# Optimization experiments

Measured on AMD Instinct MI355X. Metric: run time of the kernel, lower is better.

## Reference

```python
import jax, jax.numpy as jnp
import numpy as np

N_NODES = 100000
N_EDGES = 1600000
IN_DIM = 512
HID = 32
BN_EPS = 1e-5


def _gcn_layer(x, W, b, src, dst, n_nodes):
    # GCNConv: x' = D^{-1/2} (A + I) D^{-1/2} (x W) + b, degrees include self-loop
    h = x @ W  # [N, H]
    deg = jax.ops.segment_sum(jnp.ones(src.shape[0], x.dtype), dst, num_segments=n_nodes) + 1.0
    dinv = jax.lax.rsqrt(deg)  # [N]
    coef = dinv[src] * dinv[dst]  # [E]
    msg = h[src] * coef[:, None]  # gather + scale, [E, H]
    agg = jax.ops.segment_sum(msg, dst, num_segments=n_nodes)  # scatter-add
    agg = agg + h * (dinv * dinv)[:, None]  # self-loop term
    return agg + b


def setup_inputs() -> dict:
    key = jax.random.key(0)
    ks = jax.random.split(key, 10)
    x = jax.random.normal(ks[0], (N_NODES, IN_DIM), dtype=jnp.float32)
    edge_index = jax.random.randint(ks[1], (2, N_EDGES), 0, N_NODES, dtype=jnp.int32)
    W1 = jax.random.normal(ks[2], (IN_DIM, HID), dtype=jnp.float32) / np.sqrt(IN_DIM)
    b1 = jnp.zeros((HID,), jnp.float32)
    W2 = jax.random.normal(ks[3], (HID, HID), dtype=jnp.float32) / np.sqrt(HID)
    b2 = jnp.zeros((HID,), jnp.float32)
    gamma = jnp.ones((HID,), jnp.float32)
    beta = jnp.zeros((HID,), jnp.float32)
    run_mean = jnp.zeros((HID,), jnp.float32)
    run_var = jnp.ones((HID,), jnp.float32)
    return {"x": x, "edge_index": edge_index, "W1": W1, "b1": b1, "W2": W2,
            "b2": b2, "gamma": gamma, "beta": beta, "run_mean": run_mean, "run_var": run_var}


def reference(x, edge_index, W1, b1, W2, b2, gamma, beta, run_mean, run_var):
    # Eval mode: dropout is identity, BatchNorm uses running stats.
    src, dst = edge_index[0], edge_index[1]
    h = _gcn_layer(x, W1, b1, src, dst, N_NODES)
    h = jax.nn.relu(h)
    h = (h - run_mean) * jax.lax.rsqrt(run_var + BN_EPS) * gamma + beta
    h = _gcn_layer(h, W2, b2, src, dst, N_NODES)
    h = jax.nn.relu(h)
    return h  # post_process is undefined in source -> identity
```

## Files before the change

### kernel.cpp

```cpp
#include <hip/hip_runtime.h>

#define NN 100000
#define NE 1600000
#define IN_DIM 512
#define HID 32
#define BN_EPS 1e-5f

#define E_PER 4
#define FILL_BLOCKS 1600
#define NPASS 25
#define SEG 64

__global__ void k_zero(int* __restrict__ p, int n) {
    int i = blockIdx.x * 256 + threadIdx.x;
    if (i < n) p[i] = 0;
}

__global__ __launch_bounds__(256) void k_fill(const int* __restrict__ src,
                                              const int* __restrict__ dst,
                                              int* __restrict__ cnt,
                                              int* __restrict__ csr, int E, int nthreads) {
    int tid = blockIdx.x * 256 + threadIdx.x;
    int s[E_PER], d[E_PER];
#pragma unroll
    for (int k = 0; k < E_PER; k++) {
        int e = tid + k * nthreads;
        bool ok = (e < E);
        s[k] = ok ? src[e] : 0;
        d[k] = ok ? dst[e] : -1;
    }
    for (int p = 0; p < NPASS; p++) {
#pragma unroll
        for (int k = 0; k < E_PER; k++) {
            if ((d[k] >> 12) == p) {
                int pos = atomicAdd(&cnt[d[k]], 1);
                if (pos < SEG) csr[d[k] * SEG + pos] = s[k];
            }
        }
    }
}

__device__ inline void fma4(float4& a, float s, const float4& w) {
    a.x = fmaf(s, w.x, a.x);
    a.y = fmaf(s, w.y, a.y);
    a.z = fmaf(s, w.z, a.z);
    a.w = fmaf(s, w.w, a.w);
}

#define XS_S 132
__global__ __launch_bounds__(256) void k_gemm1(const float* __restrict__ x,
                                               const float* __restrict__ W,
                                               float* __restrict__ h, int n) {
    __shared__ float XsT[32 * XS_S];
    __shared__ float Ws[32 * 32];
    int t = threadIdx.x;
    int tc = t & 7;
    int tr = t >> 3;
    int base = blockIdx.x * 128;

    float4 acc[4] = {{0,0,0,0},{0,0,0,0},{0,0,0,0},{0,0,0,0}};
    int st_c4 = t & 7, st_row = t >> 3;

    for (int kt = 0; kt < IN_DIM; kt += 32) {
        __syncthreads();
#pragma unroll
        for (int i = 0; i < 4; i++) {
            int row = st_row + i * 32;
            int gr = min(base + row, n - 1);
            float4 v = *(const float4*)(x + (size_t)gr * IN_DIM + kt + (st_c4 << 2));
            XsT[(st_c4 * 4 + 0) * XS_S + row] = v.x;
            XsT[(st_c4 * 4 + 1) * XS_S + row] = v.y;
            XsT[(st_c4 * 4 + 2) * XS_S + row] = v.z;
            XsT[(st_c4 * 4 + 3) * XS_S + row] = v.w;
        }
        *(float4*)&Ws[t * 4] = *(const float4*)(W + kt * HID + t * 4);
        __syncthreads();

#pragma unroll
        for (int kk = 0; kk < 32; kk++) {
            float4 xv = *(const float4*)&XsT[kk * XS_S + tr * 4];
            float4 wv = *(const float4*)&Ws[kk * HID + tc * 4];
            fma4(acc[0], xv.x, wv);
            fma4(acc[1], xv.y, wv);
            fma4(acc[2], xv.z, wv);
            fma4(acc[3], xv.w, wv);
        }
    }
#pragma unroll
    for (int r = 0; r < 4; r++) {
        int row = base + tr * 4 + r;
        if (row < n) *(float4*)(h + (size_t)row * HID + (tc << 2)) = acc[r];
    }
}

__global__ __launch_bounds__(256) void k_agg1(const float* __restrict__ h,
                                              const int* __restrict__ csr,
                                              const int* __restrict__ cnt,
                                              const float* __restrict__ bias,
                                              const float* __restrict__ gamma,
                                              const float* __restrict__ beta,
                                              const float* __restrict__ mean,
                                              const float* __restrict__ var,
                                              float* __restrict__ h2, int n) {
    int t = threadIdx.x;
    int c = t & 31;
    int node = blockIdx.x * 8 + (t >> 5);
    if (node >= n) return;

    int dnode = cnt[node];
    float dn = rsqrtf((float)dnode + 1.0f);
    int d = min(dnode, SEG);
    int o0 = node * SEG;
    float sum = h[(size_t)node * HID + c] * dn;

    for (int ch = 0; ch < d; ch += 32) {
        int rem = d - ch;
        int sv = 0;
        float dv = 0.f;
        if (c < rem) {
            sv = csr[o0 + ch + c];
            dv = rsqrtf((float)cnt[sv] + 1.0f);
        }
        int m = min(rem, 32);
        int mu = (m + 7) & ~7;
        for (int j = 0; j < mu; j += 8) {
            int ss[8];
            float cf[8], v[8];
#pragma unroll
            for (int u = 0; u < 8; u++) {
                ss[u] = __shfl(sv, j + u, 32);
                cf[u] = __shfl(dv, j + u, 32);
            }
#pragma unroll
            for (int u = 0; u < 8; u++) v[u] = h[(size_t)ss[u] * HID + c];
#pragma unroll
            for (int u = 0; u < 8; u++) sum = fmaf(v[u], cf[u], sum);
        }
    }
    float acc = sum * dn;
    float v = fmaxf(acc + bias[c], 0.0f);
    v = (v - mean[c]) * rsqrtf(var[c] + BN_EPS) * gamma[c] + beta[c];
    h2[(size_t)node * HID + c] = v;
}

__global__ __launch_bounds__(256) void k_agg2(const float* __restrict__ h2,
                                              const int* __restrict__ csr,
                                              const int* __restrict__ cnt,
                                              const float* __restrict__ W2,
                                              const float* __restrict__ b2,
                                              float* __restrict__ out, int n) {
    __shared__ float W2s[32 * 32];
    int t = threadIdx.x;
    ((float4*)W2s)[t] = ((const float4*)W2)[t];
    __syncthreads();

    int c = t & 31;
    int node = blockIdx.x * 8 + (t >> 5);
    if (node >= n) return;

    int dnode = cnt[node];
    float dn = rsqrtf((float)dnode + 1.0f);
    int d = min(dnode, SEG);
    int o0 = node * SEG;
    float sum = h2[(size_t)node * HID + c] * dn;

    for (int ch = 0; ch < d; ch += 32) {
        int rem = d - ch;
        int sv = 0;
        float dv = 0.f;
        if (c < rem) {
            sv = csr[o0 + ch + c];
            dv = rsqrtf((float)cnt[sv] + 1.0f);
        }
        int m = min(rem, 32);
        int mu = (m + 7) & ~7;
        for (int j = 0; j < mu; j += 8) {
            int ss[8];
            float cf[8], v[8];
#pragma unroll
            for (int u = 0; u < 8; u++) {
                ss[u] = __shfl(sv, j + u, 32);
                cf[u] = __shfl(dv, j + u, 32);
            }
#pragma unroll
            for (int u = 0; u < 8; u++) v[u] = h2[(size_t)ss[u] * HID + c];
#pragma unroll
            for (int u = 0; u < 8; u++) sum = fmaf(v[u], cf[u], sum);
        }
    }
    float acc = sum * dn;
    float g = 0.f;
#pragma unroll
    for (int cc = 0; cc < 32; cc++) {
        float a = __shfl(acc, cc, 32);
        g = fmaf(a, W2s[cc * HID + c], g);
    }
    out[(size_t)node * HID + c] = fmaxf(g + b2[c], 0.0f);
}

extern "C" void kernel_launch(void* const* d_in, const int* in_sizes, int n_in,
                              void* d_out, int out_size, void* d_ws, size_t ws_size,
                              hipStream_t stream) {
    const float* x     = (const float*)d_in[0];
    const int*   ei    = (const int*)d_in[1];
    const int*   src   = ei;
    const int*   dst   = ei + NE;
    const float* W1    = (const float*)d_in[2];
    const float* b1    = (const float*)d_in[3];
    const float* W2    = (const float*)d_in[4];
    const float* b2    = (const float*)d_in[5];
    const float* gamma = (const float*)d_in[6];
    const float* beta  = (const float*)d_in[7];
    const float* rmean = (const float*)d_in[8];
    const float* rvar  = (const float*)d_in[9];
    float* out = (float*)d_out;

    char* ws = (char*)d_ws;
    int*   cnt = (int*)(ws);
    int*   csr = (int*)(ws + ((size_t)1 << 20));
    float* h1  = (float*)(ws + ((size_t)28 << 20));
    float* h2  = (float*)(ws + ((size_t)42 << 20));

    const int fill_threads = FILL_BLOCKS * 256;

    k_zero<<<(NN + 255) / 256, 256, 0, stream>>>(cnt, NN);
    k_fill<<<FILL_BLOCKS, 256, 0, stream>>>(src, dst, cnt, csr, NE, fill_threads);

    k_gemm1<<<(NN + 127) / 128, 256, 0, stream>>>(x, W1, h1, NN);
    k_agg1<<<(NN + 7) / 8, 256, 0, stream>>>(h1, csr, cnt, b1, gamma, beta,
                                             rmean, rvar, h2, NN);
    k_agg2<<<(NN + 7) / 8, 256, 0, stream>>>(h2, csr, cnt, W2, b2, out, NN);
}
```

Before: 485.9 us.

## Merge CSR fill and first-layer GEMM into one interleaved-block kernel

Combines the atomic-heavy CSR build and the memory-bound x@W1 GEMM into a single launch, putting a GEMM block at every third block index so the two independent workloads run on the GPU at the same time. The aim is to hide the latency-bound atomic scatter behind the bandwidth-bound GEMM and drop one launch. The trade-off is that fill blocks now carry the GEMM's shared-memory allocation and register usage, which may reduce how many fill blocks fit on each CU.

Result: faster. 464.4 us (-4.4%).

```diff
diff --git a/kernel.cpp b/kernel.cpp
--- a/kernel.cpp
+++ b/kernel.cpp
@@ -8,36 +8,14 @@
 
 #define E_PER 4
 #define FILL_BLOCKS 1600
+#define GEMM_BLOCKS 782
+#define FG_BLOCKS (FILL_BLOCKS + GEMM_BLOCKS)
 #define NPASS 25
 #define SEG 64
 
 __global__ void k_zero(int* __restrict__ p, int n) {
     int i = blockIdx.x * 256 + threadIdx.x;
     if (i < n) p[i] = 0;
-}
-
-__global__ __launch_bounds__(256) void k_fill(const int* __restrict__ src,
-                                              const int* __restrict__ dst,
-                                              int* __restrict__ cnt,
-                                              int* __restrict__ csr, int E, int nthreads) {
-    int tid = blockIdx.x * 256 + threadIdx.x;
-    int s[E_PER], d[E_PER];
-#pragma unroll
-    for (int k = 0; k < E_PER; k++) {
-        int e = tid + k * nthreads;
-        bool ok = (e < E);
-        s[k] = ok ? src[e] : 0;
-        d[k] = ok ? dst[e] : -1;
-    }
-    for (int p = 0; p < NPASS; p++) {
-#pragma unroll
-        for (int k = 0; k < E_PER; k++) {
-            if ((d[k] >> 12) == p) {
-                int pos = atomicAdd(&cnt[d[k]], 1);
-                if (pos < SEG) csr[d[k] * SEG + pos] = s[k];
-            }
-        }
-    }
 }
 
 __device__ inline void fma4(float4& a, float s, const float4& w) {
@@ -48,15 +26,47 @@
 }
 
 #define XS_S 132
-__global__ __launch_bounds__(256) void k_gemm1(const float* __restrict__ x,
-                                               const float* __restrict__ W,
-                                               float* __restrict__ h, int n) {
+__global__ __launch_bounds__(256) void k_fill_gemm(const int* __restrict__ src,
+                                                   const int* __restrict__ dst,
+                                                   int* __restrict__ cnt,
+                                                   int* __restrict__ csr,
+                                                   const float* __restrict__ x,
+                                                   const float* __restrict__ W,
+                                                   float* __restrict__ h) {
     __shared__ float XsT[32 * XS_S];
     __shared__ float Ws[32 * 32];
+    int bid = blockIdx.x;
     int t = threadIdx.x;
+    bool is_gemm = (bid % 3 == 2) && (bid / 3 < GEMM_BLOCKS);
+
+    if (!is_gemm) {
+        int f = bid - min(GEMM_BLOCKS, (bid + 1) / 3);
+        const int nthreads = FILL_BLOCKS * 256;
+        int tid = f * 256 + t;
+        int s[E_PER], d[E_PER];
+#pragma unroll
+        for (int k = 0; k < E_PER; k++) {
+            int e = tid + k * nthreads;
+            bool ok = (e < NE);
+            s[k] = ok ? src[e] : 0;
+            d[k] = ok ? dst[e] : -1;
+        }
+        for (int p = 0; p < NPASS; p++) {
+#pragma unroll
+            for (int k = 0; k < E_PER; k++) {
+                if ((d[k] >> 12) == p) {
+                    int pos = atomicAdd(&cnt[d[k]], 1);
+                    if (pos < SEG) csr[d[k] * SEG + pos] = s[k];
+                }
+            }
+        }
+        return;
+    }
+
+    int g = bid / 3;
     int tc = t & 7;
     int tr = t >> 3;
-    int base = blockIdx.x * 128;
+    int base = g * 128;
 
     float4 acc[4] = {{0,0,0,0},{0,0,0,0},{0,0,0,0},{0,0,0,0}};
     int st_c4 = t & 7, st_row = t >> 3;
@@ -66,7 +76,7 @@
 #pragma unroll
         for (int i = 0; i < 4; i++) {
             int row = st_row + i * 32;
-            int gr = min(base + row, n - 1);
+            int gr = min(base + row, NN - 1);
             float4 v = *(const float4*)(x + (size_t)gr * IN_DIM + kt + (st_c4 << 2));
             XsT[(st_c4 * 4 + 0) * XS_S + row] = v.x;
             XsT[(st_c4 * 4 + 1) * XS_S + row] = v.y;
@@ -89,7 +99,7 @@
 #pragma unroll
     for (int r = 0; r < 4; r++) {
         int row = base + tr * 4 + r;
-        if (row < n) *(float4*)(h + (size_t)row * HID + (tc << 2)) = acc[r];
+        if (row < NN) *(float4*)(h + (size_t)row * HID + (tc << 2)) = acc[r];
     }
 }
 
@@ -221,12 +231,8 @@
     float* h1  = (float*)(ws + ((size_t)28 << 20));
     float* h2  = (float*)(ws + ((size_t)42 << 20));
 
-    const int fill_threads = FILL_BLOCKS * 256;
-
     k_zero<<<(NN + 255) / 256, 256, 0, stream>>>(cnt, NN);
-    k_fill<<<FILL_BLOCKS, 256, 0, stream>>>(src, dst, cnt, csr, NE, fill_threads);
-
-    k_gemm1<<<(NN + 127) / 128, 256, 0, stream>>>(x, W1, h1, NN);
+    k_fill_gemm<<<FG_BLOCKS, 256, 0, stream>>>(src, dst, cnt, csr, x, W1, h1);
     k_agg1<<<(NN + 7) / 8, 256, 0, stream>>>(h1, csr, cnt, b1, gamma, beta,
                                              rmean, rvar, h2, NN);
     k_agg2<<<(NN + 7) / 8, 256, 0, stream>>>(h2, csr, cnt, W2, b2, out, NN);
```
